# Performance work log

Hardware: AMD Instinct MI355X
Metric: run time of the kernel (lower is better)

Reference implementation:

```python
import jax, jax.numpy as jnp
import numpy as np


def _conv(x, w, b=None, pad=0):
    # x: [N,C,H,W], w: [O,I,kh,kw]
    out = jax.lax.conv_general_dilated(
        x, w, window_strides=(1, 1), padding=[(pad, pad), (pad, pad)],
        dimension_numbers=('NCHW', 'OIHW', 'NCHW'))
    if b is not None:
        out = out + b[None, :, None, None]
    return out


def _sift128(patch):
    """Differentiable SIFT descriptor on [M,1,24,24] -> [M,128].
    Sobel gradients -> 8-bin hard-argmax orientation histogram weighted by
    gradient magnitude -> 4x4 grid of 6x6 cell sums -> L2 normalize -> **0.9."""
    sx = jnp.array([[-1., 0., 1.], [-2., 0., 2.], [-1., 0., 1.]], dtype=patch.dtype)
    gw = jnp.stack([sx, sx.T])[:, None]                     # [2,1,3,3] (Ix, Iy filters)
    g = _conv(patch, gw, pad=1)                             # [M,2,24,24]
    Ix, Iy = g[:, 0], g[:, 1]
    mag = jnp.sqrt(Ix * Ix + Iy * Iy + 1e-12)               # [M,24,24]
    ang = jnp.pi / 8 + jnp.arange(8, dtype=patch.dtype) * (jnp.pi / 4)
    # projection of gradient onto each of 8 orientation unit vectors
    cosines = (jnp.cos(ang)[None, :, None, None] * Ix[:, None]
               + jnp.sin(ang)[None, :, None, None] * Iy[:, None])  # [M,8,24,24]
    mask = (cosines == cosines.max(axis=1, keepdims=True)).astype(patch.dtype)
    hist = mask * mag[:, None]                              # [M,8,24,24] soft-binned magnitudes
    M = hist.shape[0]
    cells = hist.reshape(M, 8, 4, 6, 4, 6).sum(axis=(3, 5))  # [M,8,4,4] cell accumulation
    feat = cells.reshape(M, 128)
    feat = feat / (jnp.linalg.norm(feat, axis=1, keepdims=True) + 1e-8)
    return (feat + 1e-8) ** 0.9


def setup_inputs() -> dict:
    key = jax.random.key(0)
    ks = jax.random.split(key, 4)
    x = jax.random.normal(ks[0], (8192, 784), dtype=jnp.float32)
    W1 = jax.random.normal(ks[1], (32, 1, 3, 3), dtype=jnp.float32) * 0.1
    b1 = jnp.zeros((32,), jnp.float32)
    W2 = jax.random.normal(ks[2], (3, 32, 3, 3), dtype=jnp.float32) * 0.05
    b2 = jnp.zeros((3,), jnp.float32)
    Wl = jax.random.normal(ks[3], (10, 384), dtype=jnp.float32) * 0.05
    bl = jnp.zeros((10,), jnp.float32)
    return {"x": x, "W1": W1, "b1": b1, "W2": W2, "b2": b2, "Wl": Wl, "bl": bl}


def reference(x, W1, b1, W2, b2, Wl, bl):
    x = x.reshape(-1, 1, 28, 28)
    x = jax.nn.relu(_conv(x, W1, b1))          # [N,32,26,26]
    x = _conv(x, W2, b2)                       # [N,3,24,24]
    N = x.shape[0]
    # per-channel SIFT loop == batched SIFT over N*3 single-channel patches
    feats = _sift128(x.reshape(N * 3, 1, 24, 24)).reshape(N, 3 * 128)
    logits = feats @ Wl.T + bl                 # [N,10]
    return jax.nn.softmax(jax.nn.relu(logits), axis=1)
```

## Files before the change

kernel.cpp:

```cpp
#include <hip/hip_runtime.h>
#include <math.h>

#define TPB 576

__device__ __forceinline__ float f4c(const float4 v, int p) {
    return (p == 0) ? v.x : ((p == 1) ? v.y : v.z);
}

__global__ __launch_bounds__(TPB) void fused_pipeline(
    const float* __restrict__ x,
    const float* __restrict__ W1,
    const float* __restrict__ b1,
    const float* __restrict__ W2,
    const float* __restrict__ b2,
    const float* __restrict__ Wl,
    const float* __restrict__ bl,
    float* __restrict__ out)
{
    __shared__ __align__(16) char arena[37200];
    float4* const s2v  = (float4*)(arena);
    float*  const xs   = (float*)(arena + 10816);
    float4* const buf  = (float4*)(arena + 13952);
    float4* const pm   = (float4*)(arena + 13952);
    float*  const hist = (float*)(arena + 35584);
    float*  const nrm  = (float*)(arena + 37120);
    float*  const lg   = (float*)(arena + 37136);

    const int n = blockIdx.x;
    const int t = threadIdx.x;

    if (t < 196) ((float4*)xs)[t] = ((const float4*)(x + n * 784))[t];
    if (t < 100) {
        int idx;
        if (t < 26)      idx = t;
        else if (t < 52) idx = 650 + (t - 26);
        else if (t < 76) idx = (t - 52 + 1) * 26;
        else             idx = (t - 76 + 1) * 26 + 25;
        s2v[idx] = make_float4(0.f, 0.f, 0.f, 0.f);
    }
    __syncthreads();

    const int p0i = t / 26, p0j = t % 26;
    float xn[9];
#pragma unroll
    for (int q = 0; q < 9; ++q)
        xn[q] = xs[(p0i + q / 3) * 28 + (p0j + q % 3)];
    const int p1 = 576 + t;
    const int p1i = p1 / 26, p1j = p1 % 26;
    float xn2[9];
    if (t < 100) {
#pragma unroll
        for (int q = 0; q < 9; ++q)
            xn2[q] = xs[(p1i + q / 3) * 28 + (p1j + q % 3)];
    }

    const int i2 = t / 24, j2 = t % 24;
    float acc[3] = {0.f, 0.f, 0.f};

    const float4* const rb0 = buf + i2 * 26 + j2;
    const float4* const rb1 = rb0 + 676;
    float4* const wb0 = buf + t;
    float4* const wb1 = wb0 + 676;
    float4* const wq0 = buf + p1;
    float4* const wq1 = wq0 + 676;

    auto conv1_step = [&](int c0, float4* wdst, float4* wdst2) {
        float4 v;
        float* vp = (float*)&v;
#pragma unroll
        for (int cc = 0; cc < 4; ++cc) {
            const float* w = W1 + (c0 + cc) * 9;
            float s = b1[c0 + cc];
#pragma unroll
            for (int q = 0; q < 9; ++q) s = fmaf(w[q], xn[q], s);
            vp[cc] = fmaxf(s, 0.f);
        }
        *wdst = v;
        if (t < 100) {
            float4 v2;
            float* vp2 = (float*)&v2;
#pragma unroll
            for (int cc = 0; cc < 4; ++cc) {
                const float* w = W1 + (c0 + cc) * 9;
                float s = b1[c0 + cc];
#pragma unroll
                for (int q = 0; q < 9; ++q) s = fmaf(w[q], xn2[q], s);
                vp2[cc] = fmaxf(s, 0.f);
            }
            *wdst2 = v2;
        }
    };

    auto conv2_step = [&](int c0, const float4* r) {
#pragma unroll
        for (int di = 0; di < 3; ++di) {
            const float4 a0 = r[di * 26 + 0];
            const float4 a1 = r[di * 26 + 1];
            const float4 a2 = r[di * 26 + 2];
#pragma unroll
            for (int k = 0; k < 3; ++k) {
                const float* w = W2 + k * 288 + c0 * 9 + di * 3;
                float s = acc[k];
                s = fmaf(w[0],  a0.x, s); s = fmaf(w[9],  a0.y, s);
                s = fmaf(w[18], a0.z, s); s = fmaf(w[27], a0.w, s);
                s = fmaf(w[1],  a1.x, s); s = fmaf(w[10], a1.y, s);
                s = fmaf(w[19], a1.z, s); s = fmaf(w[28], a1.w, s);
                s = fmaf(w[2],  a2.x, s); s = fmaf(w[11], a2.y, s);
                s = fmaf(w[20], a2.z, s); s = fmaf(w[29], a2.w, s);
                acc[k] = s;
            }
        }
    };

#pragma unroll 1
    for (int cc2 = 0; cc2 < 4; ++cc2) {
        const int c0 = cc2 * 8;
        conv1_step(c0, wb0, wq0);
        __syncthreads();
        conv2_step(c0, rb0);
        conv1_step(c0 + 4, wb1, wq1);
        __syncthreads();
        conv2_step(c0 + 4, rb1);
    }

    s2v[(i2 + 1) * 26 + (j2 + 1)] =
        make_float4(acc[0] + b2[0], acc[1] + b2[1], acc[2] + b2[2], 0.f);
    __syncthreads();

    {
        const float C0c = 0.92387953f;
        const float C1c = 0.38268343f;
        const float4* P = s2v + i2 * 26 + j2;
        float4 Pr[3][3];
#pragma unroll
        for (int r = 0; r < 3; ++r)
#pragma unroll
            for (int c = 0; c < 3; ++c) Pr[r][c] = P[r * 26 + c];

        float mg[3];
        unsigned int msk = 0u;
#pragma unroll
        for (int p = 0; p < 3; ++p) {
            const float p00 = f4c(Pr[0][0], p), p01 = f4c(Pr[0][1], p), p02 = f4c(Pr[0][2], p);
            const float p10 = f4c(Pr[1][0], p),                         p12 = f4c(Pr[1][2], p);
            const float p20 = f4c(Pr[2][0], p), p21 = f4c(Pr[2][1], p), p22 = f4c(Pr[2][2], p);
            const float Ix = (p02 - p00) + 2.f * (p12 - p10) + (p22 - p20);
            const float Iy = (p20 - p00) + 2.f * (p21 - p01) + (p22 - p02);
            mg[p] = sqrtf(Ix * Ix + Iy * Iy + 1e-12f);
            float cs[8];
            cs[0] =  C0c * Ix + C1c * Iy;
            cs[1] =  C1c * Ix + C0c * Iy;
            cs[2] = -C1c * Ix + C0c * Iy;
            cs[3] = -C0c * Ix + C1c * Iy;
            cs[4] = -C0c * Ix - C1c * Iy;
            cs[5] = -C1c * Ix - C0c * Iy;
            cs[6] =  C1c * Ix - C0c * Iy;
            cs[7] =  C0c * Ix - C1c * Iy;
            float cm = cs[0];
#pragma unroll
            for (int k = 1; k < 8; ++k) cm = fmaxf(cm, cs[k]);
#pragma unroll
            for (int k = 0; k < 8; ++k)
                if (cs[k] == cm) msk |= (1u << (p * 8 + k));
        }
        pm[i2 * 25 + j2] = make_float4(mg[0], mg[1], mg[2], __uint_as_float(msk));
    }
    __syncthreads();

    if (t < 128) {
        const int k = t >> 4, cell = t & 15;
        const int r0 = (cell >> 2) * 6, c0p = (cell & 3) * 6;
        const float4* cp = pm + r0 * 25 + c0p;
        float s0 = 0.f, s1 = 0.f, s2 = 0.f;
#pragma unroll
        for (int r = 0; r < 6; ++r)
#pragma unroll
            for (int c = 0; c < 6; ++c) {
                const float4 v = cp[r * 25 + c];
                const unsigned int m = __float_as_uint(v.w);
                s0 += (m & (1u <<  k))       ? v.x : 0.f;
                s1 += (m & (1u << (8 + k)))  ? v.y : 0.f;
                s2 += (m & (1u << (16 + k))) ? v.z : 0.f;
            }
        hist[      k * 16 + cell] = s0;
        hist[128 + k * 16 + cell] = s1;
        hist[256 + k * 16 + cell] = s2;
    }
    __syncthreads();

    if (t < 192) {
        const int p = t >> 6, l = t & 63;
        const float2 v = ((const float2*)(hist + p * 128))[l];
        float s = v.x * v.x + v.y * v.y;
#pragma unroll
        for (int off = 32; off; off >>= 1) s += __shfl_down(s, off);
        if (l == 0) nrm[p] = sqrtf(s) + 1e-8f;
    }
    __syncthreads();

    if (t < 384) {
        const float v = hist[t] / nrm[t >> 7] + 1e-8f;
        hist[t] = __expf(0.9f * __logf(v));
    }
    __syncthreads();

    if (t < 160) {
        const int o = t >> 4, l = t & 15;
        const float4* hv = (const float4*)hist + l * 6;
        const float4* wv = (const float4*)(Wl + o * 384) + l * 6;
        float s = 0.f;
#pragma unroll
        for (int q = 0; q < 6; ++q) {
            const float4 h = hv[q], w = wv[q];
            s += h.x * w.x + h.y * w.y + h.z * w.z + h.w * w.w;
        }
#pragma unroll
        for (int off = 8; off; off >>= 1) s += __shfl_down(s, off, 16);
        if (l == 0) lg[o] = s + bl[o];
    }
    __syncthreads();

    if (t == 0) {
        float z[10], m = 0.f, ssum = 0.f;
#pragma unroll
        for (int o = 0; o < 10; ++o) { z[o] = fmaxf(lg[o], 0.f); m = fmaxf(m, z[o]); }
#pragma unroll
        for (int o = 0; o < 10; ++o) { z[o] = __expf(z[o] - m); ssum += z[o]; }
        const float inv = 1.f / ssum;
#pragma unroll
        for (int o = 0; o < 10; ++o) lg[o] = z[o] * inv;
    }
    __syncthreads();
    if (t < 10) out[n * 10 + t] = lg[t];
}

extern "C" void kernel_launch(void* const* d_in, const int* in_sizes, int n_in,
                              void* d_out, int out_size, void* d_ws, size_t ws_size,
                              hipStream_t stream) {
    const float* x  = (const float*)d_in[0];
    const float* W1 = (const float*)d_in[1];
    const float* b1 = (const float*)d_in[2];
    const float* W2 = (const float*)d_in[3];
    const float* b2 = (const float*)d_in[4];
    const float* Wl = (const float*)d_in[5];
    const float* bl = (const float*)d_in[6];
    float* out = (float*)d_out;
    const int N = in_sizes[0] / 784;
    fused_pipeline<<<N, TPB, 0, stream>>>(x, W1, b1, W2, b2, Wl, bl, out);
}
```

Baseline: 488.0 us.

## Recompute conv1 per output pixel in registers instead of staging through LDS

```diff
diff --git a/kernel.cpp b/kernel.cpp
--- a/kernel.cpp
+++ b/kernel.cpp
@@ -7,7 +7,7 @@
     return (p == 0) ? v.x : ((p == 1) ? v.y : v.z);
 }
 
-__global__ __launch_bounds__(TPB) void fused_pipeline(
+__global__ __launch_bounds__(TPB, 7) void fused_pipeline(
     const float* __restrict__ x,
     const float* __restrict__ W1,
     const float* __restrict__ b1,
@@ -17,14 +17,13 @@
     const float* __restrict__ bl,
     float* __restrict__ out)
 {
-    __shared__ __align__(16) char arena[37200];
+    __shared__ __align__(16) char arena[25168];
     float4* const s2v  = (float4*)(arena);
     float*  const xs   = (float*)(arena + 10816);
-    float4* const buf  = (float4*)(arena + 13952);
     float4* const pm   = (float4*)(arena + 13952);
-    float*  const hist = (float*)(arena + 35584);
-    float*  const nrm  = (float*)(arena + 37120);
-    float*  const lg   = (float*)(arena + 37136);
+    float*  const hist = (float*)(arena + 23552);
+    float*  const nrm  = (float*)(arena + 25088);
+    float*  const lg   = (float*)(arena + 25104);
 
     const int n = blockIdx.x;
     const int t = threadIdx.x;
@@ -40,87 +39,42 @@
     }
     __syncthreads();
 
-    const int p0i = t / 26, p0j = t % 26;
-    float xn[9];
-#pragma unroll
-    for (int q = 0; q < 9; ++q)
-        xn[q] = xs[(p0i + q / 3) * 28 + (p0j + q % 3)];
-    const int p1 = 576 + t;
-    const int p1i = p1 / 26, p1j = p1 % 26;
-    float xn2[9];
-    if (t < 100) {
-#pragma unroll
-        for (int q = 0; q < 9; ++q)
-            xn2[q] = xs[(p1i + q / 3) * 28 + (p1j + q % 3)];
-    }
-
     const int i2 = t / 24, j2 = t % 24;
+
+    float xw[5][5];
+#pragma unroll
+    for (int r = 0; r < 5; ++r)
+#pragma unroll
+        for (int c = 0; c < 5; ++c)
+            xw[r][c] = xs[(i2 + r) * 28 + (j2 + c)];
+
     float acc[3] = {0.f, 0.f, 0.f};
-
-    const float4* const rb0 = buf + i2 * 26 + j2;
-    const float4* const rb1 = rb0 + 676;
-    float4* const wb0 = buf + t;
-    float4* const wb1 = wb0 + 676;
-    float4* const wq0 = buf + p1;
-    float4* const wq1 = wq0 + 676;
-
-    auto conv1_step = [&](int c0, float4* wdst, float4* wdst2) {
-        float4 v;
-        float* vp = (float*)&v;
-#pragma unroll
-        for (int cc = 0; cc < 4; ++cc) {
-            const float* w = W1 + (c0 + cc) * 9;
-            float s = b1[c0 + cc];
-#pragma unroll
-            for (int q = 0; q < 9; ++q) s = fmaf(w[q], xn[q], s);
-            vp[cc] = fmaxf(s, 0.f);
+#pragma unroll 2
+    for (int ch = 0; ch < 32; ++ch) {
+        const float* w1c = W1 + ch * 9;
+        const float  b1c = b1[ch];
+        float v[9];
+#pragma unroll
+        for (int r = 0; r < 3; ++r)
+#pragma unroll
+            for (int c = 0; c < 3; ++c) {
+                float s = b1c;
+#pragma unroll
+                for (int qr = 0; qr < 3; ++qr)
+#pragma unroll
+                    for (int qc = 0; qc < 3; ++qc)
+                        s = fmaf(w1c[qr * 3 + qc], xw[r + qr][c + qc], s);
+                v[r * 3 + c] = fmaxf(s, 0.f);
+            }
+        const float* w2c = W2 + ch * 9;
+#pragma unroll
+        for (int k = 0; k < 3; ++k) {
+            const float* w = w2c + k * 288;
+            float s = acc[k];
+#pragma unroll
+            for (int q = 0; q < 9; ++q) s = fmaf(w[q], v[q], s);
+            acc[k] = s;
         }
-        *wdst = v;
-        if (t < 100) {
-            float4 v2;
-            float* vp2 = (float*)&v2;
-#pragma unroll
-            for (int cc = 0; cc < 4; ++cc) {
-                const float* w = W1 + (c0 + cc) * 9;
-                float s = b1[c0 + cc];
-#pragma unroll
-                for (int q = 0; q < 9; ++q) s = fmaf(w[q], xn2[q], s);
-                vp2[cc] = fmaxf(s, 0.f);
-            }
-            *wdst2 = v2;
-        }
-    };
-
-    auto conv2_step = [&](int c0, const float4* r) {
-#pragma unroll
-        for (int di = 0; di < 3; ++di) {
-            const float4 a0 = r[di * 26 + 0];
-            const float4 a1 = r[di * 26 + 1];
-            const float4 a2 = r[di * 26 + 2];
-#pragma unroll
-            for (int k = 0; k < 3; ++k) {
-                const float* w = W2 + k * 288 + c0 * 9 + di * 3;
-                float s = acc[k];
-                s = fmaf(w[0],  a0.x, s); s = fmaf(w[9],  a0.y, s);
-                s = fmaf(w[18], a0.z, s); s = fmaf(w[27], a0.w, s);
-                s = fmaf(w[1],  a1.x, s); s = fmaf(w[10], a1.y, s);
-                s = fmaf(w[19], a1.z, s); s = fmaf(w[28], a1.w, s);
-                s = fmaf(w[2],  a2.x, s); s = fmaf(w[11], a2.y, s);
-                s = fmaf(w[20], a2.z, s); s = fmaf(w[29], a2.w, s);
-                acc[k] = s;
-            }
-        }
-    };
-
-#pragma unroll 1
-    for (int cc2 = 0; cc2 < 4; ++cc2) {
-        const int c0 = cc2 * 8;
-        conv1_step(c0, wb0, wq0);
-        __syncthreads();
-        conv2_step(c0, rb0);
-        conv1_step(c0 + 4, wb1, wq1);
-        __syncthreads();
-        conv2_step(c0 + 4, rb1);
     }
 
     s2v[(i2 + 1) * 26 + (j2 + 1)] =
```

After: 628.1 us. 28.7% more time.
